# Kernel optimization log

Hardware: AMD Instinct MI355X
Metric: run time of the kernel (lower is better)

Reference implementation:

```python
import jax, jax.numpy as jnp
import numpy as np

B, T = 32, 32
I, H, O = 8192, 8192, 2048
NNZ_HH, NNZ_IH, NNZ_HO = 1_048_576, 524_288, 262_144


def spmm(rows, cols, vals, n_out, x):
    # COO sparse (n_out, n_in) @ x (n_in, B) -> (n_out, B).
    # Duplicate (row,col) pairs sum, matching torch_sparse.coalesce semantics.
    return jax.ops.segment_sum(vals[:, None] * x[cols], rows, num_segments=n_out)


def setup_inputs() -> dict:
    key = jax.random.key(0)
    ks = jax.random.split(key, 10)
    x = jax.random.normal(ks[0], (B, T, I), jnp.float32)
    hh_rows = jax.random.randint(ks[1], (NNZ_HH,), 0, H)
    hh_cols = jax.random.randint(ks[2], (NNZ_HH,), 0, H)
    hh_vals = jax.random.normal(ks[3], (NNZ_HH,), jnp.float32) * 0.02
    hh_bias = jnp.zeros((H, 1), jnp.float32)
    ih_rows = jax.random.randint(ks[4], (NNZ_IH,), 0, H)
    ih_cols = jax.random.randint(ks[5], (NNZ_IH,), 0, I)
    ih_vals = jax.random.normal(ks[6], (NNZ_IH,), jnp.float32) * 0.02
    ho_rows = jax.random.randint(ks[7], (NNZ_HO,), 0, O)
    ho_cols = jax.random.randint(ks[8], (NNZ_HO,), 0, H)
    ho_vals = jax.random.normal(ks[9], (NNZ_HO,), jnp.float32) * 0.02
    ho_bias = jnp.zeros((O, 1), jnp.float32)
    return dict(x=x, hh_rows=hh_rows, hh_cols=hh_cols, hh_vals=hh_vals,
                hh_bias=hh_bias, ih_rows=ih_rows, ih_cols=ih_cols,
                ih_vals=ih_vals, ho_rows=ho_rows, ho_cols=ho_cols,
                ho_vals=ho_vals, ho_bias=ho_bias)


def reference(x, hh_rows, hh_cols, hh_vals, hh_bias,
              ih_rows, ih_cols, ih_vals,
              ho_rows, ho_cols, ho_vals, ho_bias):
    # batch_first (B, T, I) -> time-major feature-first (T, I, B)
    xs = jnp.transpose(x, (1, 2, 0))
    h0 = jnp.zeros((H, B), x.dtype)  # default_hidden_init_fn='zeros'

    def step(h, x_t):
        pre = (spmm(ih_rows, ih_cols, ih_vals, H, x_t)  # ih (bias_ih=False)
               + spmm(hh_rows, hh_cols, hh_vals, H, h)
               + hh_bias)
        h_new = jax.nn.sigmoid(pre)  # nonlinearity='Sigmoid'
        out_t = spmm(ho_rows, ho_cols, ho_vals, O, h_new) + ho_bias
        return h_new, out_t

    _, outs = jax.lax.scan(step, h0, xs)  # outs: (T, O, B)
    return jnp.transpose(outs, (2, 0, 1))  # (B, T, O)
```

## Files before the change

### kernel.cpp

```cpp
#include <hip/hip_runtime.h>
#include <hip/hip_fp16.h>

constexpr int Bb = 32;
constexpr int Tt = 32;
constexpr int Ii = 8192;
constexpr int Hh = 8192;
constexpr int Oo = 2048;
constexpr int TB = Tt * Bb;
constexpr int TCH = 4;
constexpr int TILE = 2048;
constexpr int FBR = 32;
constexpr int NFB_H = Hh / FBR;
constexpr int NFB_O = Oo / FBR;


__device__ __forceinline__ float entval(uint32_t u) {
  return __half2float(__ushort_as_half((unsigned short)(u >> 16)));
}

__global__ void transpose_x_kernel(const float* __restrict__ x, __half2* __restrict__ x2) {
  int blk = blockIdx.x;
  int tp = blk >> 7;
  int ib = blk & 127;
  int t0 = tp * 2;
  int i0 = ib * 64;
  __shared__ float lds[64][65];
  int tid = threadIdx.x;
  for (int idx = tid; idx < 64 * 64; idx += 256) {
    int row = idx >> 6, il = idx & 63;
    int tt = row >> 5, bb = row & 31;
    lds[il][row] = x[(size_t)bb * Tt * Ii + (size_t)(t0 + tt) * Ii + i0 + il];
  }
  __syncthreads();
  for (int idx = tid; idx < 64 * 32; idx += 256) {
    int il = idx >> 5;
    int q = idx & 31;
    int tt = q >> 4, p = q & 15;
    float lo = lds[il][tt * 32 + 2 * p];
    float hi = lds[il][tt * 32 + 2 * p + 1];
    x2[(size_t)(i0 + il) * (TB / 2) + (size_t)(t0 + tt) * 16 + p] = __floats2half2_rn(lo, hi);
  }
}

__global__ void __launch_bounds__(256) count_kernel(
    const int* __restrict__ r1, int n1, int* __restrict__ tb1, int nt1,
    const int* __restrict__ r2, int n2, int* __restrict__ tb2, int nt2,
    const int* __restrict__ r3, int n3, int* __restrict__ tb3) {
  __shared__ int cnt[NFB_H];
  int tile = blockIdx.x;
  const int* rows; int n; int* tb; int tl; int nfb;
  if (tile < nt1)            { rows = r1; n = n1; tb = tb1; tl = tile;             nfb = NFB_H; }
  else if (tile < nt1 + nt2) { rows = r2; n = n2; tb = tb2; tl = tile - nt1;       nfb = NFB_H; }
  else                       { rows = r3; n = n3; tb = tb3; tl = tile - nt1 - nt2; nfb = NFB_O; }
  for (int i = threadIdx.x; i < nfb; i += 256) cnt[i] = 0;
  __syncthreads();
  int base = tl * TILE;
  for (int k = threadIdx.x; k < TILE; k += 256) {
    int j = base + k;
    if (j < n) atomicAdd(&cnt[rows[j] >> 5], 1);
  }
  __syncthreads();
  for (int i = threadIdx.x; i < nfb; i += 256) tb[tl * nfb + i] = cnt[i];
}

__global__ void __launch_bounds__(256) scan_col_kernel(
    int* __restrict__ tb1, int nt1, int* __restrict__ tb2, int nt2,
    int* __restrict__ tb3, int nt3, int* __restrict__ totals) {
  __shared__ int sums[256];
  int col = blockIdx.x;
  int* tb; int nt; int fb; int nfb;
  if (col < NFB_H)          { tb = tb1; nt = nt1; fb = col;             nfb = NFB_H; }
  else if (col < 2 * NFB_H) { tb = tb2; nt = nt2; fb = col - NFB_H;     nfb = NFB_H; }
  else                      { tb = tb3; nt = nt3; fb = col - 2 * NFB_H; nfb = NFB_O; }
  int tid = threadIdx.x;
  int nper = (nt + 255) >> 8;
  int vals[8];
  int t0 = tid * nper;
  int a = 0;
  for (int i = 0; i < nper; i++) {
    int t = t0 + i;
    vals[i] = (t < nt) ? tb[t * nfb + fb] : 0;
    a += vals[i];
  }
  sums[tid] = a;
  __syncthreads();
  for (int off = 1; off < 256; off <<= 1) {
    int o = (tid >= off) ? sums[tid - off] : 0;
    __syncthreads();
    sums[tid] += o;
    __syncthreads();
  }
  int run = sums[tid] - a;
  for (int i = 0; i < nper; i++) {
    int t = t0 + i;
    if (t < nt) { tb[t * nfb + fb] = run; run += vals[i]; }
  }
  if (tid == 255) totals[col] = sums[255];
}

__global__ void __launch_bounds__(256) scan_base_kernel(
    const int* __restrict__ totals, int* __restrict__ fbb1,
    int* __restrict__ fbb2, int* __restrict__ fbb3) {
  __shared__ int s[256];
  int m = blockIdx.x;
  const int* t; int* fbb; int nfb;
  if (m == 0)      { t = totals;             fbb = fbb1; nfb = NFB_H; }
  else if (m == 1) { t = totals + NFB_H;     fbb = fbb2; nfb = NFB_H; }
  else             { t = totals + 2 * NFB_H; fbb = fbb3; nfb = NFB_O; }
  int tid = threadIdx.x;
  int v = (tid < nfb) ? t[tid] : 0;
  s[tid] = v;
  __syncthreads();
  for (int off = 1; off < 256; off <<= 1) {
    int o = (tid >= off) ? s[tid - off] : 0;
    __syncthreads();
    s[tid] += o;
    __syncthreads();
  }
  if (tid < nfb) fbb[tid] = s[tid] - v;
  if (tid == 255) fbb[nfb] = s[255];
}

__global__ void __launch_bounds__(256) place_kernel(
    const int* __restrict__ r1, const int* __restrict__ c1, const float* __restrict__ v1,
    int n1, const int* __restrict__ tb1, int nt1, const int* __restrict__ fbb1, uint64_t* __restrict__ s1,
    const int* __restrict__ r2, const int* __restrict__ c2, const float* __restrict__ v2,
    int n2, const int* __restrict__ tb2, int nt2, const int* __restrict__ fbb2, uint64_t* __restrict__ s2,
    const int* __restrict__ r3, const int* __restrict__ c3, const float* __restrict__ v3,
    int n3, const int* __restrict__ tb3, const int* __restrict__ fbb3, uint64_t* __restrict__ s3) {
  __shared__ int cnt[NFB_H];
  __shared__ int incl[NFB_H];
  __shared__ uint64_t stg[TILE];
  __shared__ int gad[TILE];
  int tile = blockIdx.x;
  const int* rows; const int* cols; const float* vals; int n;
  const int* tb; const int* fbb; uint64_t* st; int tl; int nfb;
  if (tile < nt1)            { rows = r1; cols = c1; vals = v1; n = n1; tb = tb1; fbb = fbb1; st = s1; tl = tile;             nfb = NFB_H; }
  else if (tile < nt1 + nt2) { rows = r2; cols = c2; vals = v2; n = n2; tb = tb2; fbb = fbb2; st = s2; tl = tile - nt1;       nfb = NFB_H; }
  else                       { rows = r3; cols = c3; vals = v3; n = n3; tb = tb3; fbb = fbb3; st = s3; tl = tile - nt1 - nt2; nfb = NFB_O; }
  int tid = threadIdx.x;
  for (int i = tid; i < NFB_H; i += 256) cnt[i] = 0;
  __syncthreads();
  constexpr int E = TILE / 256;
  uint32_t entv[E]; int rowv[E]; int rnkv[E];
  int base = tl * TILE;
  for (int k = 0; k < E; k++) {
    int j = base + k * 256 + tid;
    if (j < n) {
      int rr = rows[j];
      rowv[k] = rr;
      entv[k] = ((uint32_t)__half_as_ushort(__float2half_rn(vals[j])) << 16) | (uint32_t)cols[j];
      rnkv[k] = atomicAdd(&cnt[rr >> 5], 1);
    } else {
      rowv[k] = -1;
    }
  }
  __syncthreads();
  int v0 = cnt[tid];
  incl[tid] = v0;
  __syncthreads();
  for (int off = 1; off < 256; off <<= 1) {
    int o = (tid >= off) ? incl[tid - off] : 0;
    __syncthreads();
    incl[tid] += o;
    __syncthreads();
  }
  int total = incl[255];
  for (int k = 0; k < E; k++) {
    if (rowv[k] >= 0) {
      int fb = rowv[k] >> 5;
      int slot = (incl[fb] - cnt[fb]) + rnkv[k];
      stg[slot] = ((uint64_t)entv[k] << 32) | (uint32_t)rowv[k];
      gad[slot] = fbb[fb] + tb[tl * nfb + fb] + rnkv[k];
    }
  }
  __syncthreads();
  for (int i = tid; i < total; i += 256) st[gad[i]] = stg[i];
}

__global__ void __launch_bounds__(256) rowcount_kernel(
    const uint64_t* __restrict__ s1, const int* __restrict__ fbb1, int* __restrict__ cu1,
    const uint64_t* __restrict__ s2, const int* __restrict__ fbb2, int* __restrict__ cu2,
    const uint64_t* __restrict__ s3, const int* __restrict__ fbb3, int* __restrict__ cu3) {
  __shared__ int rc[FBR];
  int bx = blockIdx.x;
  const uint64_t* st; const int* fbb; int* cu; int b;
  if (bx < NFB_H)          { st = s1; fbb = fbb1; cu = cu1; b = bx; }
  else if (bx < 2 * NFB_H) { st = s2; fbb = fbb2; cu = cu2; b = bx - NFB_H; }
  else                     { st = s3; fbb = fbb3; cu = cu3; b = bx - 2 * NFB_H; }
  int tid = threadIdx.x;
  if (tid < FBR) rc[tid] = 0;
  __syncthreads();
  int lo = fbb[b], hi = fbb[b + 1];
  for (int j = lo + tid; j < hi; j += 256)
    atomicAdd(&rc[(int)(uint32_t)st[j] & (FBR - 1)], 1);
  __syncthreads();
  if (tid < FBR) cu[(b << 5) + tid] = rc[tid];
}

__global__ void scan_csr_kernel(int* __restrict__ c1, int n1, int* __restrict__ r1,
                                int* __restrict__ c2, int n2, int* __restrict__ r2,
                                int* __restrict__ c3, int n3, int* __restrict__ r3) {
  __shared__ int sums[1024];
  int bx = blockIdx.x;
  int tid = threadIdx.x;
  int* cnt_cursor; int n; int* row_start;
  if (bx == 0)      { cnt_cursor = c1; n = n1; row_start = r1; }
  else if (bx == 1) { cnt_cursor = c2; n = n2; row_start = r2; }
  else              { cnt_cursor = c3; n = n3; row_start = r3; }
  int chunk = (n + 1023) >> 10;
  int base = tid * chunk;
  int s = 0;
  for (int i = 0; i < chunk; i++) {
    int idx = base + i;
    if (idx < n) s += (cnt_cursor[idx] + 15) & ~15;
  }
  sums[tid] = s;
  __syncthreads();
  for (int off = 1; off < 1024; off <<= 1) {
    int other = (tid >= off) ? sums[tid - off] : 0;
    __syncthreads();
    sums[tid] += other;
    __syncthreads();
  }
  int run = sums[tid] - s;
  for (int i = 0; i < chunk; i++) {
    int idx = base + i;
    if (idx < n) {
      int v = cnt_cursor[idx];
      row_start[idx] = run;
      cnt_cursor[idx] = run + v;
      run += (v + 15) & ~15;
    }
  }
  if (tid == 1023) row_start[n] = sums[1023];
}

__global__ void __launch_bounds__(256) csort_kernel(
    const uint64_t* __restrict__ s1, const int* __restrict__ fbb1, const int* __restrict__ rs1, uint32_t* __restrict__ e1,
    const uint64_t* __restrict__ s2, const int* __restrict__ fbb2, const int* __restrict__ rs2, uint32_t* __restrict__ e2,
    const uint64_t* __restrict__ s3, const int* __restrict__ fbb3, const int* __restrict__ rs3, uint32_t* __restrict__ e3) {
  __shared__ uint32_t ob[8192];
  __shared__ int rcnt[FBR];
  __shared__ int rsl[FBR + 1];
  int bx = blockIdx.x;
  const uint64_t* st; const int* fbb; const int* rs; uint32_t* e; int b;
  if (bx < NFB_H)            { st = s1; fbb = fbb1; rs = rs1; e = e1; b = bx; }
  else if (bx < 2 * NFB_H)   { st = s2; fbb = fbb2; rs = rs2; e = e2; b = bx - NFB_H; }
  else                       { st = s3; fbb = fbb3; rs = rs3; e = e3; b = bx - 2 * NFB_H; }
  int tid = threadIdx.x;
  if (tid <= FBR) rsl[tid] = rs[(b << 5) + tid];
  if (tid < FBR) rcnt[tid] = 0;
  __syncthreads();
  int reg0 = rsl[0];
  int rlen = rsl[FBR] - reg0;
  int lo = fbb[b], hi = fbb[b + 1];
  if (rlen <= 8192) {
    for (int i = tid; i < rlen; i += 256) ob[i] = 0;
    __syncthreads();
    for (int j = lo + tid; j < hi; j += 256) {
      uint64_t v = st[j];
      int rl = (int)(uint32_t)v & (FBR - 1);
      int rk = atomicAdd(&rcnt[rl], 1);
      ob[(rsl[rl] - reg0) + rk] = (uint32_t)(v >> 32);
    }
    __syncthreads();
    for (int i = tid; i < rlen; i += 256) e[reg0 + i] = ob[i];
  } else {
    for (int i = tid; i < rlen; i += 256) e[reg0 + i] = 0;
    __syncthreads();
    for (int j = lo + tid; j < hi; j += 256) {
      uint64_t v = st[j];
      int rl = (int)(uint32_t)v & (FBR - 1);
      int rk = atomicAdd(&rcnt[rl], 1);
      e[rsl[rl] + rk] = (uint32_t)(v >> 32);
    }
  }
}

__global__ void __launch_bounds__(256, 8) preih_kernel(
    const int* __restrict__ ih_rs, const int* __restrict__ ih_cur,
    const uint32_t* __restrict__ ih_ent,
    const float* __restrict__ hh_bias, const __half* __restrict__ x2h,
    __half2* __restrict__ preAll) {
  int xcd = blockIdx.x & 7;
  int r = ((blockIdx.x >> 3) << 2) + (threadIdx.x >> 6);
  int lane = threadIdx.x & 63;
  int t0 = xcd * TCH;
  int s0  = __builtin_amdgcn_readfirstlane(ih_rs[r]);
  int cnt = __builtin_amdgcn_readfirstlane(ih_cur[r]) - s0;
  int nb = (cnt + 7) >> 3;
  const int4* ep = (const int4*)(ih_ent + s0);
  const uint32_t* xb = (const uint32_t*)(x2h + (size_t)t0 * Bb);

  float2 a0 = {0.f, 0.f}, a1 = {0.f, 0.f}, a2 = {0.f, 0.f}, a3 = {0.f, 0.f};
  int4 f0 = ep[0], f1 = ep[1];
  for (int i = 0; i < nb; i++) {
    int4 e0 = f0, e1 = f1;
    f0 = ep[2 * i + 2];
    f1 = ep[2 * i + 3];
    uint32_t u0 = (uint32_t)e0.x, u1 = (uint32_t)e0.y, u2 = (uint32_t)e0.z, u3 = (uint32_t)e0.w;
    uint32_t u4 = (uint32_t)e1.x, u5 = (uint32_t)e1.y, u6 = (uint32_t)e1.z, u7 = (uint32_t)e1.w;
    uint32_t g0 = xb[(size_t)(u0 & 0xffff) * (TB / 2) + lane];
    uint32_t g1 = xb[(size_t)(u1 & 0xffff) * (TB / 2) + lane];
    uint32_t g2 = xb[(size_t)(u2 & 0xffff) * (TB / 2) + lane];
    uint32_t g3 = xb[(size_t)(u3 & 0xffff) * (TB / 2) + lane];
    uint32_t g4 = xb[(size_t)(u4 & 0xffff) * (TB / 2) + lane];
    uint32_t g5 = xb[(size_t)(u5 & 0xffff) * (TB / 2) + lane];
    uint32_t g6 = xb[(size_t)(u6 & 0xffff) * (TB / 2) + lane];
    uint32_t g7 = xb[(size_t)(u7 & 0xffff) * (TB / 2) + lane];
    float v0 = entval(u0), v1 = entval(u1), v2 = entval(u2), v3 = entval(u3);
    float v4 = entval(u4), v5 = entval(u5), v6 = entval(u6), v7 = entval(u7);
    float2 x0 = __half22float2(*(__half2*)&g0), x1 = __half22float2(*(__half2*)&g1);
    float2 x2v = __half22float2(*(__half2*)&g2), x3 = __half22float2(*(__half2*)&g3);
    float2 x4 = __half22float2(*(__half2*)&g4), x5 = __half22float2(*(__half2*)&g5);
    float2 x6 = __half22float2(*(__half2*)&g6), x7 = __half22float2(*(__half2*)&g7);
    a0.x += v0 * x0.x;  a0.y += v0 * x0.y;   a0.x += v4 * x4.x;  a0.y += v4 * x4.y;
    a1.x += v1 * x1.x;  a1.y += v1 * x1.y;   a1.x += v5 * x5.x;  a1.y += v5 * x5.y;
    a2.x += v2 * x2v.x; a2.y += v2 * x2v.y;  a2.x += v6 * x6.x;  a2.y += v6 * x6.y;
    a3.x += v3 * x3.x;  a3.y += v3 * x3.y;   a3.x += v7 * x7.x;  a3.y += v7 * x7.y;
  }
  float bias = hh_bias[r];
  float sx = ((a0.x + a1.x) + (a2.x + a3.x)) + bias;
  float sy = ((a0.y + a1.y) + (a2.y + a3.y)) + bias;
  int tt = lane >> 4, p = lane & 15;
  preAll[((size_t)(t0 + tt) * Hh + r) * 16 + p] = __floats2half2_rn(sx, sy);
}

__global__ void __launch_bounds__(256, 8) step_kernel(
    const int* __restrict__ hh_rs, const int* __restrict__ hh_cur,
    const uint32_t* __restrict__ hh_ent,
    const __half* __restrict__ pre_t,
    const __half* __restrict__ hprev,
    __half* __restrict__ hnext) {
  int r = (blockIdx.x * 256 + threadIdx.x) >> 6;
  int lane = threadIdx.x & 63;
  int q = lane >> 4, p = lane & 15;
  int s0  = __builtin_amdgcn_readfirstlane(hh_rs[r]);
  int cnt = __builtin_amdgcn_readfirstlane(hh_cur[r]) - s0;
  int nb = (cnt + 15) >> 4;
  const int4* ep = (const int4*)(hh_ent + s0);
  const uint32_t* hp = (const uint32_t*)hprev;
  uint32_t pu = ((const uint32_t*)pre_t)[(r << 4) + p];
  float2 pre2 = __half22float2(*(__half2*)&pu);

  float2 a0 = {0.f, 0.f}, a1 = {0.f, 0.f};
  int4 f = ep[q];
  for (int i = 0; i < nb; i++) {
    int4 e = f;
    f = ep[4 * (i + 1) + q];
    uint32_t u0 = (uint32_t)e.x, u1 = (uint32_t)e.y, u2 = (uint32_t)e.z, u3 = (uint32_t)e.w;
    uint32_t g0 = hp[((u0 & 0xffff) << 4) + p];
    uint32_t g1 = hp[((u1 & 0xffff) << 4) + p];
    uint32_t g2 = hp[((u2 & 0xffff) << 4) + p];
    uint32_t g3 = hp[((u3 & 0xffff) << 4) + p];
    float v0 = entval(u0), v1 = entval(u1), v2 = entval(u2), v3 = entval(u3);
    float2 x0 = __half22float2(*(__half2*)&g0), x1 = __half22float2(*(__half2*)&g1);
    float2 x2v = __half22float2(*(__half2*)&g2), x3 = __half22float2(*(__half2*)&g3);
    a0.x += v0 * x0.x;  a0.y += v0 * x0.y;
    a1.x += v1 * x1.x;  a1.y += v1 * x1.y;
    a0.x += v2 * x2v.x; a0.y += v2 * x2v.y;
    a1.x += v3 * x3.x;  a1.y += v3 * x3.y;
  }
  float ax = a0.x + a1.x, ay = a0.y + a1.y;
  ax += __shfl_xor(ax, 16, 64);  ay += __shfl_xor(ay, 16, 64);
  ax += __shfl_xor(ax, 32, 64);  ay += __shfl_xor(ay, 32, 64);
  float hv0 = 1.0f / (1.0f + __expf(-(pre2.x + ax)));
  float hv1 = 1.0f / (1.0f + __expf(-(pre2.y + ay)));
  if (q == 0) ((__half2*)hnext)[(r << 4) + p] = __floats2half2_rn(hv0, hv1);
}

__global__ void __launch_bounds__(256, 8) out_kernel(
    const int* __restrict__ ho_rs, const int* __restrict__ ho_cur,
    const uint32_t* __restrict__ ho_ent,
    const float* __restrict__ ho_bias, const __half* __restrict__ hAll,
    float* __restrict__ out_tmp) {
  int xcd = blockIdx.x & 7;
  int w   = (blockIdx.x >> 3) * 4 + (threadIdx.x >> 6);
  int lane = threadIdx.x & 63;
  int h = lane >> 5, b = lane & 31;
  int t0 = xcd * 4;
  constexpr size_t HS = (size_t)Hh * Bb;
  const __half* hbase = hAll + (size_t)(t0 + 1) * HS;

  for (int o = w; o < Oo; o += 1024) {
    int s0  = __builtin_amdgcn_readfirstlane(ho_rs[o]);
    int cnt = __builtin_amdgcn_readfirstlane(ho_cur[o]) - s0;
    int nb = (cnt + 7) >> 3;
    const int4* ep = (const int4*)(ho_ent + s0);
    float bias = (h == 0) ? ho_bias[o] : 0.f;
    float A0 = bias, A1 = bias, A2 = bias, A3 = bias;
    float B0 = 0.f, B1 = 0.f, B2 = 0.f, B3 = 0.f;
    for (int i = 0; i < nb; i++) {
      int4 e0 = ep[2 * i], e1 = ep[2 * i + 1];
      uint32_t u0 = (uint32_t)(h ? e0.y : e0.x);
      uint32_t u1 = (uint32_t)(h ? e0.w : e0.z);
      uint32_t u2 = (uint32_t)(h ? e1.y : e1.x);
      uint32_t u3 = (uint32_t)(h ? e1.w : e1.z);
      const __half* p0 = hbase + (((size_t)(u0 & 0xffff)) << 5) + b;
      const __half* p1 = hbase + (((size_t)(u1 & 0xffff)) << 5) + b;
      const __half* p2 = hbase + (((size_t)(u2 & 0xffff)) << 5) + b;
      const __half* p3 = hbase + (((size_t)(u3 & 0xffff)) << 5) + b;
      float v0 = entval(u0), v1 = entval(u1), v2 = entval(u2), v3 = entval(u3);
      A0 += v0 * __half2float(p0[0]);
      A1 += v0 * __half2float(p0[HS]);
      A2 += v0 * __half2float(p0[2 * HS]);
      A3 += v0 * __half2float(p0[3 * HS]);
      B0 += v1 * __half2float(p1[0]);
      B1 += v1 * __half2float(p1[HS]);
      B2 += v1 * __half2float(p1[2 * HS]);
      B3 += v1 * __half2float(p1[3 * HS]);
      A0 += v2 * __half2float(p2[0]);
      A1 += v2 * __half2float(p2[HS]);
      A2 += v2 * __half2float(p2[2 * HS]);
      A3 += v2 * __half2float(p2[3 * HS]);
      B0 += v3 * __half2float(p3[0]);
      B1 += v3 * __half2float(p3[HS]);
      B2 += v3 * __half2float(p3[2 * HS]);
      B3 += v3 * __half2float(p3[3 * HS]);
    }
    A0 += B0; A1 += B1; A2 += B2; A3 += B3;
    A0 += __shfl_xor(A0, 32, 64);
    A1 += __shfl_xor(A1, 32, 64);
    A2 += __shfl_xor(A2, 32, 64);
    A3 += __shfl_xor(A3, 32, 64);
    if (h == 0) {
      out_tmp[((size_t)(t0 + 0) * Oo + o) * Bb + b] = A0;
      out_tmp[((size_t)(t0 + 1) * Oo + o) * Bb + b] = A1;
      out_tmp[((size_t)(t0 + 2) * Oo + o) * Bb + b] = A2;
      out_tmp[((size_t)(t0 + 3) * Oo + o) * Bb + b] = A3;
    }
  }
}

__global__ void transpose_out_kernel(const float* __restrict__ out_tmp, float* __restrict__ dout) {
  int blk = blockIdx.x;
  int t  = blk >> 5;
  int o0 = (blk & 31) << 6;
  __shared__ float lds[64][33];
  int tid = threadIdx.x;
  for (int idx = tid; idx < 64 * 32; idx += 256) {
    int ol = idx >> 5, bb = idx & 31;
    lds[ol][bb] = out_tmp[(size_t)t * Oo * Bb + (size_t)(o0 + ol) * Bb + bb];
  }
  __syncthreads();
  for (int idx = tid; idx < 32 * 64; idx += 256) {
    int bb = idx >> 6, ol = idx & 63;
    dout[(size_t)bb * Tt * Oo + (size_t)t * Oo + o0 + ol] = lds[ol][bb];
  }
}

extern "C" void kernel_launch(void* const* d_in, const int* in_sizes, int n_in,
                              void* d_out, int out_size, void* d_ws, size_t ws_size,
                              hipStream_t stream) {
  const float* x       = (const float*)d_in[0];
  const int*   hh_rows = (const int*)d_in[1];
  const int*   hh_cols = (const int*)d_in[2];
  const float* hh_vals = (const float*)d_in[3];
  const float* hh_bias = (const float*)d_in[4];
  const int*   ih_rows = (const int*)d_in[5];
  const int*   ih_cols = (const int*)d_in[6];
  const float* ih_vals = (const float*)d_in[7];
  const int*   ho_rows = (const int*)d_in[8];
  const int*   ho_cols = (const int*)d_in[9];
  const float* ho_vals = (const float*)d_in[10];
  const float* ho_bias = (const float*)d_in[11];
  float* out = (float*)d_out;

  const int nnz_hh = in_sizes[1];
  const int nnz_ih = in_sizes[5];
  const int nnz_ho = in_sizes[8];

  const int ntile_ih = (nnz_ih + TILE - 1) / TILE;
  const int ntile_hh = (nnz_hh + TILE - 1) / TILE;
  const int ntile_ho = (nnz_ho + TILE - 1) / TILE;

  char* w = (char*)d_ws;
  size_t off = 0;
  auto alloc = [&](size_t bytes) -> void* {
    void* p = w + off;
    off += (bytes + 255) & ~(size_t)255;
    return p;
  };
  __half* x2h    = (__half*)alloc(2 * (size_t)Ii * TB);
  __half* hAll   = (__half*)alloc(2 * (size_t)(Tt + 1) * Hh * Bb);
  __half* preAll = (__half*)alloc(2 * (size_t)Tt * Hh * Bb);
  float* out_tmp = (float*)alloc(4 * (size_t)Tt * Oo * Bb);
  int*  ih_rs  = (int*)alloc(4 * (size_t)(Hh + 1));
  int*  hh_rs  = (int*)alloc(4 * (size_t)(Hh + 1));
  int*  ho_rs  = (int*)alloc(4 * (size_t)(Oo + 1));
  int*  cur_all = (int*)alloc(4 * (size_t)(Hh + Hh + Oo));
  int*  ih_cur = cur_all;
  int*  hh_cur = cur_all + Hh;
  int*  ho_cur = cur_all + 2 * Hh;
  uint32_t* ih_ent = (uint32_t*)alloc(4 * ((size_t)nnz_ih + 16 * Hh + 64));
  uint32_t* hh_ent = (uint32_t*)alloc(4 * ((size_t)nnz_hh + 16 * Hh + 64));
  uint32_t* ho_ent = (uint32_t*)alloc(4 * ((size_t)nnz_ho + 16 * Oo + 64));
  int* tb_ih  = (int*)alloc(4 * (size_t)(ntile_ih * NFB_H));
  int* tb_hh  = (int*)alloc(4 * (size_t)(ntile_hh * NFB_H));
  int* tb_ho  = (int*)alloc(4 * (size_t)(ntile_ho * NFB_O));
  int* fbb_ih = (int*)alloc(4 * (size_t)(NFB_H + 1));
  int* fbb_hh = (int*)alloc(4 * (size_t)(NFB_H + 1));
  int* fbb_ho = (int*)alloc(4 * (size_t)(NFB_O + 1));
  int* totals = (int*)alloc(4 * (size_t)(2 * NFB_H + NFB_O));

  uint64_t* s_ih = (uint64_t*)preAll;
  uint64_t* s_hh = s_ih + (size_t)nnz_ih;
  uint64_t* s_ho = s_hh + (size_t)nnz_hh;

  hipMemsetAsync(hAll, 0, 2 * (size_t)Hh * Bb, stream);

  transpose_x_kernel<<<(Tt / 2) * (Ii / 64), 256, 0, stream>>>(x, (__half2*)x2h);

  count_kernel<<<ntile_ih + ntile_hh + ntile_ho, 256, 0, stream>>>(
      ih_rows, nnz_ih, tb_ih, ntile_ih,
      hh_rows, nnz_hh, tb_hh, ntile_hh,
      ho_rows, nnz_ho, tb_ho);
  scan_col_kernel<<<2 * NFB_H + NFB_O, 256, 0, stream>>>(
      tb_ih, ntile_ih, tb_hh, ntile_hh, tb_ho, ntile_ho, totals);
  scan_base_kernel<<<3, 256, 0, stream>>>(totals, fbb_ih, fbb_hh, fbb_ho);
  place_kernel<<<ntile_ih + ntile_hh + ntile_ho, 256, 0, stream>>>(
      ih_rows, ih_cols, ih_vals, nnz_ih, tb_ih, ntile_ih, fbb_ih, s_ih,
      hh_rows, hh_cols, hh_vals, nnz_hh, tb_hh, ntile_hh, fbb_hh, s_hh,
      ho_rows, ho_cols, ho_vals, nnz_ho, tb_ho, fbb_ho, s_ho);
  rowcount_kernel<<<2 * NFB_H + NFB_O, 256, 0, stream>>>(
      s_ih, fbb_ih, ih_cur, s_hh, fbb_hh, hh_cur, s_ho, fbb_ho, ho_cur);
  scan_csr_kernel<<<3, 1024, 0, stream>>>(
      ih_cur, Hh, ih_rs, hh_cur, Hh, hh_rs, ho_cur, Oo, ho_rs);
  csort_kernel<<<2 * NFB_H + NFB_O, 256, 0, stream>>>(
      s_ih, fbb_ih, ih_rs, ih_ent,
      s_hh, fbb_hh, hh_rs, hh_ent,
      s_ho, fbb_ho, ho_rs, ho_ent);

  preih_kernel<<<8 * Hh / 4, 256, 0, stream>>>(
      ih_rs, ih_cur, ih_ent, hh_bias, x2h, (__half2*)preAll);

  for (int t = 0; t < Tt; t++) {
    step_kernel<<<Hh / 4, 256, 0, stream>>>(
        hh_rs, hh_cur, hh_ent,
        preAll + (size_t)t * Hh * Bb,
        hAll + (size_t)t * Hh * Bb,
        hAll + (size_t)(t + 1) * Hh * Bb);
  }

  out_kernel<<<2048, 256, 0, stream>>>(
      ho_rs, ho_cur, ho_ent, ho_bias, hAll, out_tmp);
  transpose_out_kernel<<<Tt * (Oo / 64), 256, 0, stream>>>(out_tmp, out);

  (void)n_in; (void)out_size; (void)ws_size;
}
```

Before: 534.2 us.

## Widen step-kernel unroll to 8 entries and repack out-kernel lanes as half2

Row padding in the CSR scan grows from 16 to 32 entries. The recurrent step kernel now consumes 32 entries per iteration, with two int4 prefetches and eight gathers in flight per lane, to expose more memory-level parallelism. The output kernel is remapped so that 4 groups of 16 lanes each read half2 pairs of the batch instead of 2 groups of 32 lanes reading single halves. This halves the gather instruction count and adds vectorized float2 stores. The cost is more padding entries, so more wasted work on short rows, and higher register pressure.

After: 529.4 us, median of 2. Within noise of the previous version (-0.9%).

```diff
diff --git a/kernel.cpp b/kernel.cpp
--- a/kernel.cpp
+++ b/kernel.cpp
@@ -213,7 +213,7 @@
   int s = 0;
   for (int i = 0; i < chunk; i++) {
     int idx = base + i;
-    if (idx < n) s += (cnt_cursor[idx] + 15) & ~15;
+    if (idx < n) s += (cnt_cursor[idx] + 31) & ~31;
   }
   sums[tid] = s;
   __syncthreads();
@@ -230,7 +230,7 @@
       int v = cnt_cursor[idx];
       row_start[idx] = run;
       cnt_cursor[idx] = run + v;
-      run += (v + 15) & ~15;
+      run += (v + 31) & ~31;
     }
   }
   if (tid == 1023) row_start[n] = sums[1023];
@@ -338,31 +338,41 @@
   int q = lane >> 4, p = lane & 15;
   int s0  = __builtin_amdgcn_readfirstlane(hh_rs[r]);
   int cnt = __builtin_amdgcn_readfirstlane(hh_cur[r]) - s0;
-  int nb = (cnt + 15) >> 4;
+  int nb = (cnt + 31) >> 5;
   const int4* ep = (const int4*)(hh_ent + s0);
   const uint32_t* hp = (const uint32_t*)hprev;
   uint32_t pu = ((const uint32_t*)pre_t)[(r << 4) + p];
   float2 pre2 = __half22float2(*(__half2*)&pu);
 
-  float2 a0 = {0.f, 0.f}, a1 = {0.f, 0.f};
-  int4 f = ep[q];
+  float2 a0 = {0.f, 0.f}, a1 = {0.f, 0.f}, a2 = {0.f, 0.f}, a3 = {0.f, 0.f};
+  int4 fa = ep[q], fb = ep[q + 4];
   for (int i = 0; i < nb; i++) {
-    int4 e = f;
-    f = ep[4 * (i + 1) + q];
-    uint32_t u0 = (uint32_t)e.x, u1 = (uint32_t)e.y, u2 = (uint32_t)e.z, u3 = (uint32_t)e.w;
+    int4 ea = fa, eb = fb;
+    fa = ep[8 * (i + 1) + q];
+    fb = ep[8 * (i + 1) + q + 4];
+    uint32_t u0 = (uint32_t)ea.x, u1 = (uint32_t)ea.y, u2 = (uint32_t)ea.z, u3 = (uint32_t)ea.w;
+    uint32_t u4 = (uint32_t)eb.x, u5 = (uint32_t)eb.y, u6 = (uint32_t)eb.z, u7 = (uint32_t)eb.w;
     uint32_t g0 = hp[((u0 & 0xffff) << 4) + p];
     uint32_t g1 = hp[((u1 & 0xffff) << 4) + p];
     uint32_t g2 = hp[((u2 & 0xffff) << 4) + p];
     uint32_t g3 = hp[((u3 & 0xffff) << 4) + p];
+    uint32_t g4 = hp[((u4 & 0xffff) << 4) + p];
+    uint32_t g5 = hp[((u5 & 0xffff) << 4) + p];
+    uint32_t g6 = hp[((u6 & 0xffff) << 4) + p];
+    uint32_t g7 = hp[((u7 & 0xffff) << 4) + p];
     float v0 = entval(u0), v1 = entval(u1), v2 = entval(u2), v3 = entval(u3);
+    float v4 = entval(u4), v5 = entval(u5), v6 = entval(u6), v7 = entval(u7);
     float2 x0 = __half22float2(*(__half2*)&g0), x1 = __half22float2(*(__half2*)&g1);
     float2 x2v = __half22float2(*(__half2*)&g2), x3 = __half22float2(*(__half2*)&g3);
-    a0.x += v0 * x0.x;  a0.y += v0 * x0.y;
-    a1.x += v1 * x1.x;  a1.y += v1 * x1.y;
-    a0.x += v2 * x2v.x; a0.y += v2 * x2v.y;
-    a1.x += v3 * x3.x;  a1.y += v3 * x3.y;
-  }
-  float ax = a0.x + a1.x, ay = a0.y + a1.y;
+    float2 x4 = __half22float2(*(__half2*)&g4), x5 = __half22float2(*(__half2*)&g5);
+    float2 x6 = __half22float2(*(__half2*)&g6), x7 = __half22float2(*(__half2*)&g7);
+    a0.x += v0 * x0.x;  a0.y += v0 * x0.y;   a0.x += v4 * x4.x;  a0.y += v4 * x4.y;
+    a1.x += v1 * x1.x;  a1.y += v1 * x1.y;   a1.x += v5 * x5.x;  a1.y += v5 * x5.y;
+    a2.x += v2 * x2v.x; a2.y += v2 * x2v.y;  a2.x += v6 * x6.x;  a2.y += v6 * x6.y;
+    a3.x += v3 * x3.x;  a3.y += v3 * x3.y;   a3.x += v7 * x7.x;  a3.y += v7 * x7.y;
+  }
+  float ax = (a0.x + a1.x) + (a2.x + a3.x);
+  float ay = (a0.y + a1.y) + (a2.y + a3.y);
   ax += __shfl_xor(ax, 16, 64);  ay += __shfl_xor(ay, 16, 64);
   ax += __shfl_xor(ax, 32, 64);  ay += __shfl_xor(ay, 32, 64);
   float hv0 = 1.0f / (1.0f + __expf(-(pre2.x + ax)));
@@ -378,57 +388,79 @@
   int xcd = blockIdx.x & 7;
   int w   = (blockIdx.x >> 3) * 4 + (threadIdx.x >> 6);
   int lane = threadIdx.x & 63;
-  int h = lane >> 5, b = lane & 31;
+  int q = lane >> 4, p = lane & 15;
   int t0 = xcd * 4;
-  constexpr size_t HS = (size_t)Hh * Bb;
-  const __half* hbase = hAll + (size_t)(t0 + 1) * HS;
+  constexpr int HU = Hh * 16;
+  const uint32_t* hb = (const uint32_t*)hAll + (size_t)(t0 + 1) * HU;
 
   for (int o = w; o < Oo; o += 1024) {
     int s0  = __builtin_amdgcn_readfirstlane(ho_rs[o]);
     int cnt = __builtin_amdgcn_readfirstlane(ho_cur[o]) - s0;
-    int nb = (cnt + 7) >> 3;
+    int nb = (cnt + 15) >> 4;
     const int4* ep = (const int4*)(ho_ent + s0);
-    float bias = (h == 0) ? ho_bias[o] : 0.f;
-    float A0 = bias, A1 = bias, A2 = bias, A3 = bias;
-    float B0 = 0.f, B1 = 0.f, B2 = 0.f, B3 = 0.f;
+    float2 A0 = {0.f, 0.f}, A1 = {0.f, 0.f}, A2 = {0.f, 0.f}, A3 = {0.f, 0.f};
+    int4 f = ep[q];
     for (int i = 0; i < nb; i++) {
-      int4 e0 = ep[2 * i], e1 = ep[2 * i + 1];
-      uint32_t u0 = (uint32_t)(h ? e0.y : e0.x);
-      uint32_t u1 = (uint32_t)(h ? e0.w : e0.z);
-      uint32_t u2 = (uint32_t)(h ? e1.y : e1.x);
-      uint32_t u3 = (uint32_t)(h ? e1.w : e1.z);
-      const __half* p0 = hbase + (((size_t)(u0 & 0xffff)) << 5) + b;
-      const __half* p1 = hbase + (((size_t)(u1 & 0xffff)) << 5) + b;
-      const __half* p2 = hbase + (((size_t)(u2 & 0xffff)) << 5) + b;
-      const __half* p3 = hbase + (((size_t)(u3 & 0xffff)) << 5) + b;
+      int4 e = f;
+      f = ep[4 * (i + 1) + q];
+      uint32_t u0 = (uint32_t)e.x, u1 = (uint32_t)e.y, u2 = (uint32_t)e.z, u3 = (uint32_t)e.w;
+      int b0 = (int)((u0 & 0xffff) << 4) + p;
+      int b1 = (int)((u1 & 0xffff) << 4) + p;
+      int b2 = (int)((u2 & 0xffff) << 4) + p;
+      int b3 = (int)((u3 & 0xffff) << 4) + p;
       float v0 = entval(u0), v1 = entval(u1), v2 = entval(u2), v3 = entval(u3);
-      A0 += v0 * __half2float(p0[0]);
-      A1 += v0 * __half2float(p0[HS]);
-      A2 += v0 * __half2float(p0[2 * HS]);
-      A3 += v0 * __half2float(p0[3 * HS]);
-      B0 += v1 * __half2float(p1[0]);
-      B1 += v1 * __half2float(p1[HS]);
-      B2 += v1 * __half2float(p1[2 * HS]);
-      B3 += v1 * __half2float(p1[3 * HS]);
-      A0 += v2 * __half2float(p2[0]);
-      A1 += v2 * __half2float(p2[HS]);
-      A2 += v2 * __half2float(p2[2 * HS]);
-      A3 += v2 * __half2float(p2[3 * HS]);
-      B0 += v3 * __half2float(p3[0]);
-      B1 += v3 * __half2float(p3[HS]);
-      B2 += v3 * __half2float(p3[2 * HS]);
-      B3 += v3 * __half2float(p3[3 * HS]);
-    }
-    A0 += B0; A1 += B1; A2 += B2; A3 += B3;
-    A0 += __shfl_xor(A0, 32, 64);
-    A1 += __shfl_xor(A1, 32, 64);
-    A2 += __shfl_xor(A2, 32, 64);
-    A3 += __shfl_xor(A3, 32, 64);
-    if (h == 0) {
-      out_tmp[((size_t)(t0 + 0) * Oo + o) * Bb + b] = A0;
-      out_tmp[((size_t)(t0 + 1) * Oo + o) * Bb + b] = A1;
-      out_tmp[((size_t)(t0 + 2) * Oo + o) * Bb + b] = A2;
-      out_tmp[((size_t)(t0 + 3) * Oo + o) * Bb + b] = A3;
+      {
+        uint32_t g0 = hb[b0], g1 = hb[b0 + HU], g2 = hb[b0 + 2 * HU], g3 = hb[b0 + 3 * HU];
+        float2 x0 = __half22float2(*(__half2*)&g0), x1 = __half22float2(*(__half2*)&g1);
+        float2 x2v = __half22float2(*(__half2*)&g2), x3 = __half22float2(*(__half2*)&g3);
+        A0.x += v0 * x0.x;  A0.y += v0 * x0.y;
+        A1.x += v0 * x1.x;  A1.y += v0 * x1.y;
+        A2.x += v0 * x2v.x; A2.y += v0 * x2v.y;
+        A3.x += v0 * x3.x;  A3.y += v0 * x3.y;
+      }
+      {
+        uint32_t g0 = hb[b1], g1 = hb[b1 + HU], g2 = hb[b1 + 2 * HU], g3 = hb[b1 + 3 * HU];
+        float2 x0 = __half22float2(*(__half2*)&g0), x1 = __half22float2(*(__half2*)&g1);
+        float2 x2v = __half22float2(*(__half2*)&g2), x3 = __half22float2(*(__half2*)&g3);
+        A0.x += v1 * x0.x;  A0.y += v1 * x0.y;
+        A1.x += v1 * x1.x;  A1.y += v1 * x1.y;
+        A2.x += v1 * x2v.x; A2.y += v1 * x2v.y;
+        A3.x += v1 * x3.x;  A3.y += v1 * x3.y;
+      }
+      {
+        uint32_t g0 = hb[b2], g1 = hb[b2 + HU], g2 = hb[b2 + 2 * HU], g3 = hb[b2 + 3 * HU];
+        float2 x0 = __half22float2(*(__half2*)&g0), x1 = __half22float2(*(__half2*)&g1);
+        float2 x2v = __half22float2(*(__half2*)&g2), x3 = __half22float2(*(__half2*)&g3);
+        A0.x += v2 * x0.x;  A0.y += v2 * x0.y;
+        A1.x += v2 * x1.x;  A1.y += v2 * x1.y;
+        A2.x += v2 * x2v.x; A2.y += v2 * x2v.y;
+        A3.x += v2 * x3.x;  A3.y += v2 * x3.y;
+      }
+      {
+        uint32_t g0 = hb[b3], g1 = hb[b3 + HU], g2 = hb[b3 + 2 * HU], g3 = hb[b3 + 3 * HU];
+        float2 x0 = __half22float2(*(__half2*)&g0), x1 = __half22float2(*(__half2*)&g1);
+        float2 x2v = __half22float2(*(__half2*)&g2), x3 = __half22float2(*(__half2*)&g3);
+        A0.x += v3 * x0.x;  A0.y += v3 * x0.y;
+        A1.x += v3 * x1.x;  A1.y += v3 * x1.y;
+        A2.x += v3 * x2v.x; A2.y += v3 * x2v.y;
+        A3.x += v3 * x3.x;  A3.y += v3 * x3.y;
+      }
+    }
+    A0.x += __shfl_xor(A0.x, 16, 64);  A0.y += __shfl_xor(A0.y, 16, 64);
+    A1.x += __shfl_xor(A1.x, 16, 64);  A1.y += __shfl_xor(A1.y, 16, 64);
+    A2.x += __shfl_xor(A2.x, 16, 64);  A2.y += __shfl_xor(A2.y, 16, 64);
+    A3.x += __shfl_xor(A3.x, 16, 64);  A3.y += __shfl_xor(A3.y, 16, 64);
+    A0.x += __shfl_xor(A0.x, 32, 64);  A0.y += __shfl_xor(A0.y, 32, 64);
+    A1.x += __shfl_xor(A1.x, 32, 64);  A1.y += __shfl_xor(A1.y, 32, 64);
+    A2.x += __shfl_xor(A2.x, 32, 64);  A2.y += __shfl_xor(A2.y, 32, 64);
+    A3.x += __shfl_xor(A3.x, 32, 64);  A3.y += __shfl_xor(A3.y, 32, 64);
+    if (q == 0) {
+      float bias = ho_bias[o];
+      float2* ot = (float2*)out_tmp;
+      ot[(((size_t)(t0 + 0) * Oo + o) * Bb >> 1) + p] = {A0.x + bias, A0.y + bias};
+      ot[(((size_t)(t0 + 1) * Oo + o) * Bb >> 1) + p] = {A1.x + bias, A1.y + bias};
+      ot[(((size_t)(t0 + 2) * Oo + o) * Bb >> 1) + p] = {A2.x + bias, A2.y + bias};
+      ot[(((size_t)(t0 + 3) * Oo + o) * Bb >> 1) + p] = {A3.x + bias, A3.y + bias};
     }
   }
 }
@@ -493,9 +525,9 @@
   int*  ih_cur = cur_all;
   int*  hh_cur = cur_all + Hh;
   int*  ho_cur = cur_all + 2 * Hh;
-  uint32_t* ih_ent = (uint32_t*)alloc(4 * ((size_t)nnz_ih + 16 * Hh + 64));
-  uint32_t* hh_ent = (uint32_t*)alloc(4 * ((size_t)nnz_hh + 16 * Hh + 64));
-  uint32_t* ho_ent = (uint32_t*)alloc(4 * ((size_t)nnz_ho + 16 * Oo + 64));
+  uint32_t* ih_ent = (uint32_t*)alloc(4 * ((size_t)nnz_ih + 32 * Hh + 128));
+  uint32_t* hh_ent = (uint32_t*)alloc(4 * ((size_t)nnz_hh + 32 * Hh + 128));
+  uint32_t* ho_ent = (uint32_t*)alloc(4 * ((size_t)nnz_ho + 32 * Oo + 128));
   int* tb_ih  = (int*)alloc(4 * (size_t)(ntile_ih * NFB_H));
   int* tb_hh  = (int*)alloc(4 * (size_t)(ntile_hh * NFB_H));
   int* tb_ho  = (int*)alloc(4 * (size_t)(ntile_ho * NFB_O));
```
